# Kernel tuning notes

Hardware: AMD Instinct MI355X
Metric: run time of the kernel (lower is better)

## Reference

```python
import jax, jax.numpy as jnp
import numpy as np

NEG = -9e15

def setup_inputs() -> dict:
    key = jax.random.key(0)
    k1, k2, k3, k4 = jax.random.split(key, 4)
    N, F_IN, F_OUT = 8192, 256, 256
    h = jax.random.normal(k1, (N, F_IN), dtype=jnp.float32)
    adj = jax.random.randint(k2, (N, N), 0, 2, dtype=jnp.int32)
    W = jax.random.normal(k3, (F_IN, F_OUT), dtype=jnp.float32) * (1.0 / np.sqrt(F_IN))
    a = jax.random.normal(k4, (2 * F_OUT,), dtype=jnp.float32) * (1.0 / np.sqrt(2 * F_OUT))
    return {"h": h, "adj": adj, "W": W, "a": a}

def reference(h, adj, W, a):
    # Wh: [N, F_out]
    Wh = h @ W
    F_OUT = Wh.shape[1]
    a1, a2 = a[:F_OUT], a[F_OUT:]
    # cat-based score decomposes: e_ij = leaky_relu(a1.Wh_i + a2.Wh_j)
    s1 = Wh @ a1  # [N]
    s2 = Wh @ a2  # [N]
    e = jax.nn.leaky_relu(s1[:, None] + s2[None, :], negative_slope=0.2)  # [N, N]
    e = jnp.where(adj > 0, e, NEG)
    attention = jax.nn.softmax(e, axis=-1)
    # dropout is identity in eval mode
    return attention @ Wh
```

## Files before the change

kernel.cpp:

```cpp
#include <hip/hip_runtime.h>

typedef short s8v  __attribute__((ext_vector_type(8)));
typedef float f4v  __attribute__((ext_vector_type(4)));
typedef int   v4i  __attribute__((ext_vector_type(4)));
typedef float v4f  __attribute__((ext_vector_type(4)));

#define NNODES 8192
#define FDIM   256
#define NJC    4
#define JLEN   2048
#define TROWS  64
#define KSTEP  32
#define NSTEP  64

__device__ __forceinline__ float bf2f(unsigned short u) {
    unsigned int x = ((unsigned int)u) << 16;
    return __builtin_bit_cast(float, x);
}
__device__ __forceinline__ unsigned short f2bf(float f) {
    unsigned int x = __builtin_bit_cast(unsigned int, f);
    x += 0x7fffu + ((x >> 16) & 1u);
    return (unsigned short)(x >> 16);
}

__global__ __launch_bounds__(256) void wt_kernel(const float* __restrict__ W,
                                                 unsigned short* __restrict__ WT) {
    int idx = blockIdx.x * 256 + threadIdx.x;
    int r = idx >> 8, c = idx & 255;
    WT[c * 256 + r] = f2bf(W[r * 256 + c]);
}

__global__ __launch_bounds__(256) void wv_kernel(const float* __restrict__ W,
                                                 const float* __restrict__ a,
                                                 float* __restrict__ v1, float* __restrict__ v2) {
    __shared__ float r1[256], r2[256];
    int b = blockIdx.x, n = threadIdx.x;
    float w = W[(size_t)b * FDIM + n];
    r1[n] = w * a[n];
    r2[n] = w * a[FDIM + n];
    __syncthreads();
    for (int off = 128; off > 0; off >>= 1) {
        if (n < off) { r1[n] += r1[n + off]; r2[n] += r2[n + off]; }
        __syncthreads();
    }
    if (n == 0) { v1[b] = r1[0]; v2[b] = r2[0]; }
}

__global__ __launch_bounds__(256) void wh_kernel(
    const float* __restrict__ h, const unsigned short* __restrict__ WT,
    const float* __restrict__ v1, const float* __restrict__ v2,
    unsigned short* __restrict__ PB,
    float* __restrict__ s1, float* __restrict__ s2)
{
    __shared__ float v1_lds[FDIM], v2_lds[FDIM];
    int tid = threadIdx.x;
    v1_lds[tid] = v1[tid];
    v2_lds[tid] = v2[tid];
    __syncthreads();

    int w = tid >> 6, lane = tid & 63, q = lane >> 4, l15 = lane & 15;
    int i_base = blockIdx.x * 64 + w * 16;

    f4v acc[16] = {};
    float s1p = 0.f, s2p = 0.f;

    for (int k0 = 0; k0 < 256; k0 += 32) {
        const float* hp = h + (size_t)(i_base + l15) * FDIM + k0 + q * 8;
        f4v h0 = *(const f4v*)hp;
        f4v h1 = *(const f4v*)(hp + 4);
        s8v af;
#pragma unroll
        for (int j = 0; j < 4; ++j) {
            af[j]     = (short)f2bf(h0[j]);
            af[4 + j] = (short)f2bf(h1[j]);
            s1p += h0[j] * v1_lds[k0 + q * 8 + j] + h1[j] * v1_lds[k0 + q * 8 + 4 + j];
            s2p += h0[j] * v2_lds[k0 + q * 8 + j] + h1[j] * v2_lds[k0 + q * 8 + 4 + j];
        }
#pragma unroll
        for (int t = 0; t < 16; ++t) {
            s8v bf = *(const s8v*)(WT + (size_t)(t * 16 + l15) * FDIM + k0 + q * 8);
            acc[t] = __builtin_amdgcn_mfma_f32_16x16x32_bf16(af, bf, acc[t], 0, 0, 0);
        }
    }

    s1p += __shfl_xor(s1p, 16, 64);
    s1p += __shfl_xor(s1p, 32, 64);
    s2p += __shfl_xor(s2p, 16, 64);
    s2p += __shfl_xor(s2p, 32, 64);
    if (lane < 16) {
        s1[i_base + lane] = s1p;
        s2[i_base + lane] = s2p;
    }

#pragma unroll
    for (int t = 0; t < 16; ++t)
#pragma unroll
        for (int r = 0; r < 4; ++r) {
            int i = i_base + q * 4 + r;
            size_t a16 = (size_t)((i >> 5) * 16 + t) * 512
                       + l15 * 32 + ((i >> 3) & 3) * 8 + (i & 7);
            PB[a16] = f2bf(acc[t][r]);
        }
}

__global__ __launch_bounds__(256, 3) void attn_partial(
    const int* __restrict__ adj, const unsigned short* __restrict__ PB,
    const float* __restrict__ s1, const float* __restrict__ s2,
    float* __restrict__ Npart, float* __restrict__ dpart)
{
    __shared__ float s2_lds[JLEN];
    __shared__ unsigned short P_lds[2][TROWS * KSTEP];
    __shared__ float dsum_lds[TROWS][4];

    int tid = threadIdx.x;
    int rt = blockIdx.x & 127, jc = blockIdx.x >> 7;
    int j0 = jc * JLEN;

    for (int i = tid; i < JLEN / 4; i += 256)
        ((v4f*)s2_lds)[i] = ((const v4f*)(s2 + j0))[i];

    int m = tid >> 2, idx = tid & 3;
    int row_g = rt * TROWS + m;
    float s1v = s1[row_g];
    const int* arow = adj + (size_t)row_g * NNODES + j0 + idx * 8;
    int woff = ((idx * 64 + m) * 8) ^ (idx * 16);

    int g = tid >> 6, lane = tid & 63, q = lane >> 4, l15 = lane & 15;
    const unsigned short* pbb = PB + (size_t)(jc * 64) * 16 * 512 + l15 * 32 + q * 8;

    f4v acc[4][4] = {};
    float dsum = 0.0f;

    __syncthreads();

    v4i a0 = __builtin_nontemporal_load((const v4i*)(arow));
    v4i a1 = __builtin_nontemporal_load((const v4i*)(arow + 4));
    v4i cur0 = __builtin_nontemporal_load((const v4i*)(arow + KSTEP));
    v4i cur1 = __builtin_nontemporal_load((const v4i*)(arow + KSTEP + 4));
    {
        int kb = idx * 8;
        v4f sA = *(const v4f*)&s2_lds[kb];
        v4f sB = *(const v4f*)&s2_lds[kb + 4];
        s8v pv;
#pragma unroll
        for (int j = 0; j < 4; ++j) {
            float x = s1v + sA[j];
            float p = (a0[j] > 0) ? __expf(fmaxf(x, 0.2f * x)) : 0.0f;
            unsigned short pb = f2bf(p);
            pv[j] = (short)pb; dsum += bf2f(pb);
            float x2 = s1v + sB[j];
            float p2 = (a1[j] > 0) ? __expf(fmaxf(x2, 0.2f * x2)) : 0.0f;
            unsigned short pb2 = f2bf(p2);
            pv[4 + j] = (short)pb2; dsum += bf2f(pb2);
        }
        *(s8v*)&P_lds[0][woff] = pv;
    }
    __syncthreads();

    for (int s = 0; s < NSTEP; ++s) {
        int kn = (s < NSTEP - 2) ? (s + 2) * KSTEP : 0;
        v4i nx0 = __builtin_nontemporal_load((const v4i*)(arow + kn));
        v4i nx1 = __builtin_nontemporal_load((const v4i*)(arow + kn + 4));

        s8v bf[4];
#pragma unroll
        for (int t = 0; t < 4; ++t)
            bf[t] = *(const s8v*)(pbb + (size_t)(s * 16 + g * 4 + t) * 512);

        if (s < NSTEP - 1) {
            int kb = (s + 1) * KSTEP + idx * 8;
            v4f sA = *(const v4f*)&s2_lds[kb];
            v4f sB = *(const v4f*)&s2_lds[kb + 4];
            s8v pv;
#pragma unroll
            for (int j = 0; j < 4; ++j) {
                float x = s1v + sA[j];
                float p = (cur0[j] > 0) ? __expf(fmaxf(x, 0.2f * x)) : 0.0f;
                unsigned short pb = f2bf(p);
                pv[j] = (short)pb; dsum += bf2f(pb);
                float x2 = s1v + sB[j];
                float p2 = (cur1[j] > 0) ? __expf(fmaxf(x2, 0.2f * x2)) : 0.0f;
                unsigned short pb2 = f2bf(p2);
                pv[4 + j] = (short)pb2; dsum += bf2f(pb2);
            }
            *(s8v*)&P_lds[(s + 1) & 1][woff] = pv;
        }

        const unsigned short* pbuf = P_lds[s & 1];
#pragma unroll
        for (int rh = 0; rh < 4; ++rh) {
            s8v af = *(const s8v*)&pbuf[((q * 64 + rh * 16 + l15) * 8) ^ (q * 16)];
#pragma unroll
            for (int t = 0; t < 4; ++t)
                acc[rh][t] = __builtin_amdgcn_mfma_f32_16x16x32_bf16(af, bf[t], acc[rh][t], 0, 0, 0);
        }

        __syncthreads();
        cur0 = nx0; cur1 = nx1;
    }

    dsum_lds[m][idx] = dsum;
    __syncthreads();
    if (tid < TROWS) {
        float d = dsum_lds[tid][0] + dsum_lds[tid][1] + dsum_lds[tid][2] + dsum_lds[tid][3];
        dpart[jc * NNODES + rt * TROWS + tid] = d;
    }

#pragma unroll
    for (int rh = 0; rh < 4; ++rh)
#pragma unroll
        for (int r = 0; r < 4; ++r) {
            int row = rh * 16 + q * 4 + r;
            float* base = Npart + ((size_t)(jc * NNODES) + rt * TROWS + row) * FDIM;
#pragma unroll
            for (int t = 0; t < 4; ++t)
                __builtin_nontemporal_store(acc[rh][t][r], base + g * 64 + t * 16 + l15);
        }
}

__global__ __launch_bounds__(256) void reduce_kernel(
    const float* __restrict__ Npart, const float* __restrict__ dpart,
    float* __restrict__ out)
{
    int i = blockIdx.x, n = threadIdx.x;
    float d = 0.f, acc = 0.f;
#pragma unroll
    for (int jc = 0; jc < NJC; ++jc) {
        d += dpart[jc * NNODES + i];
        acc += Npart[((size_t)(jc * NNODES) + i) * FDIM + n];
    }
    out[(size_t)i * FDIM + n] = acc / fmaxf(d, 1e-30f);
}

extern "C" void kernel_launch(void* const* d_in, const int* in_sizes, int n_in,
                              void* d_out, int out_size, void* d_ws, size_t ws_size,
                              hipStream_t stream) {
    const float* h   = (const float*)d_in[0];
    const int*   adj = (const int*)d_in[1];
    const float* W   = (const float*)d_in[2];
    const float* a   = (const float*)d_in[3];
    float* out = (float*)d_out;

    char* ws = (char*)d_ws;
    unsigned short* PB = (unsigned short*)ws;
    float* s1 = (float*)(ws + (4u << 20));
    float* s2 = (float*)(ws + (4u << 20) + (32u << 10));
    unsigned short* WT = (unsigned short*)(ws + (4u << 20) + (64u << 10));
    float* v1 = (float*)(ws + (4u << 20) + (192u << 10));
    float* v2 = (float*)(ws + (4u << 20) + (193u << 10));
    float* dpart = (float*)(ws + (5u << 20));
    float* Npart = (float*)(ws + (8u << 20));

    hipLaunchKernelGGL(wt_kernel, dim3(256), dim3(256), 0, stream, W, WT);
    hipLaunchKernelGGL(wv_kernel, dim3(256), dim3(256), 0, stream, W, a, v1, v2);
    hipLaunchKernelGGL(wh_kernel, dim3(128), dim3(256), 0, stream, h, WT, v1, v2, PB, s1, s2);
    hipLaunchKernelGGL(attn_partial, dim3(128 * NJC), dim3(256), 0, stream,
                       adj, PB, s1, s2, Npart, dpart);
    hipLaunchKernelGGL(reduce_kernel, dim3(NNODES), dim3(256), 0, stream, Npart, dpart, out);
}
```

Measured before the change: 447.0 us.

## Use packed bf16 conversion, split j-range into 8 chunks, raise occupancy

Replaces the manual round-to-nearest bf16 conversion with the hardware packed v_cvt_pk_bf16_f32 instruction in both the projection and attention kernels, and writes PB as packed 2x32-bit stores. The attention kernel now splits the column range into 8 chunks of 1024 instead of 4 of 2048, reorders the block index so neighbouring blocks share a row tile, and raises launch bounds to 4 blocks per SM. The denominator now sums unrounded fp32 probabilities, so it no longer matches the bf16 values fed to the MFMA exactly. More j-chunks also mean more partial results to reduce later, and the unseen reduction code must handle NJC=8.

Measured after the change: 466.8 us. 1.04x slower.

```diff
diff --git a/kernel.cpp b/kernel.cpp
--- a/kernel.cpp
+++ b/kernel.cpp
@@ -4,14 +4,15 @@
 typedef float f4v  __attribute__((ext_vector_type(4)));
 typedef int   v4i  __attribute__((ext_vector_type(4)));
 typedef float v4f  __attribute__((ext_vector_type(4)));
+typedef int   v2i  __attribute__((ext_vector_type(2)));
 
 #define NNODES 8192
 #define FDIM   256
-#define NJC    4
-#define JLEN   2048
+#define NJC    8
+#define JLEN   1024
 #define TROWS  64
 #define KSTEP  32
-#define NSTEP  64
+#define NSTEP  32
 
 __device__ __forceinline__ float bf2f(unsigned short u) {
     unsigned int x = ((unsigned int)u) << 16;
@@ -21,6 +22,11 @@
     unsigned int x = __builtin_bit_cast(unsigned int, f);
     x += 0x7fffu + ((x >> 16) & 1u);
     return (unsigned short)(x >> 16);
+}
+__device__ __forceinline__ int cvt_pk(float lo, float hi) {
+    int r;
+    asm("v_cvt_pk_bf16_f32 %0, %1, %2" : "=v"(r) : "v"(lo), "v"(hi));
+    return r;
 }
 
 __global__ __launch_bounds__(256) void wt_kernel(const float* __restrict__ W,
@@ -68,18 +74,20 @@
         const float* hp = h + (size_t)(i_base + l15) * FDIM + k0 + q * 8;
         f4v h0 = *(const f4v*)hp;
         f4v h1 = *(const f4v*)(hp + 4);
-        s8v af;
+        union { v4i u; s8v s; } af;
+        af.u[0] = cvt_pk(h0[0], h0[1]);
+        af.u[1] = cvt_pk(h0[2], h0[3]);
+        af.u[2] = cvt_pk(h1[0], h1[1]);
+        af.u[3] = cvt_pk(h1[2], h1[3]);
 #pragma unroll
         for (int j = 0; j < 4; ++j) {
-            af[j]     = (short)f2bf(h0[j]);
-            af[4 + j] = (short)f2bf(h1[j]);
             s1p += h0[j] * v1_lds[k0 + q * 8 + j] + h1[j] * v1_lds[k0 + q * 8 + 4 + j];
             s2p += h0[j] * v2_lds[k0 + q * 8 + j] + h1[j] * v2_lds[k0 + q * 8 + 4 + j];
         }
 #pragma unroll
         for (int t = 0; t < 16; ++t) {
             s8v bf = *(const s8v*)(WT + (size_t)(t * 16 + l15) * FDIM + k0 + q * 8);
-            acc[t] = __builtin_amdgcn_mfma_f32_16x16x32_bf16(af, bf, acc[t], 0, 0, 0);
+            acc[t] = __builtin_amdgcn_mfma_f32_16x16x32_bf16(af.s, bf, acc[t], 0, 0, 0);
         }
     }
 
@@ -93,17 +101,18 @@
     }
 
 #pragma unroll
-    for (int t = 0; t < 16; ++t)
-#pragma unroll
-        for (int r = 0; r < 4; ++r) {
-            int i = i_base + q * 4 + r;
-            size_t a16 = (size_t)((i >> 5) * 16 + t) * 512
-                       + l15 * 32 + ((i >> 3) & 3) * 8 + (i & 7);
-            PB[a16] = f2bf(acc[t][r]);
-        }
-}
-
-__global__ __launch_bounds__(256, 3) void attn_partial(
+    for (int t = 0; t < 16; ++t) {
+        int i0 = i_base + q * 4;
+        size_t a16 = (size_t)((i0 >> 5) * 16 + t) * 512
+                   + l15 * 32 + ((i0 >> 3) & 3) * 8 + (i0 & 7);
+        v2i pk;
+        pk[0] = cvt_pk(acc[t][0], acc[t][1]);
+        pk[1] = cvt_pk(acc[t][2], acc[t][3]);
+        *(v2i*)(PB + a16) = pk;
+    }
+}
+
+__global__ __launch_bounds__(256, 4) void attn_partial(
     const int* __restrict__ adj, const unsigned short* __restrict__ PB,
     const float* __restrict__ s1, const float* __restrict__ s2,
     float* __restrict__ Npart, float* __restrict__ dpart)
@@ -113,7 +122,7 @@
     __shared__ float dsum_lds[TROWS][4];
 
     int tid = threadIdx.x;
-    int rt = blockIdx.x & 127, jc = blockIdx.x >> 7;
+    int jc = blockIdx.x & 7, rt = blockIdx.x >> 3;
     int j0 = jc * JLEN;
 
     for (int i = tid; i < JLEN / 4; i += 256)
@@ -126,7 +135,7 @@
     int woff = ((idx * 64 + m) * 8) ^ (idx * 16);
 
     int g = tid >> 6, lane = tid & 63, q = lane >> 4, l15 = lane & 15;
-    const unsigned short* pbb = PB + (size_t)(jc * 64) * 16 * 512 + l15 * 32 + q * 8;
+    const unsigned short* pbb = PB + (size_t)(jc * 32) * 16 * 512 + l15 * 32 + q * 8;
 
     f4v acc[4][4] = {};
     float dsum = 0.0f;
@@ -141,19 +150,22 @@
         int kb = idx * 8;
         v4f sA = *(const v4f*)&s2_lds[kb];
         v4f sB = *(const v4f*)&s2_lds[kb + 4];
-        s8v pv;
+        float pa[4], pb_[4];
 #pragma unroll
         for (int j = 0; j < 4; ++j) {
             float x = s1v + sA[j];
             float p = (a0[j] > 0) ? __expf(fmaxf(x, 0.2f * x)) : 0.0f;
-            unsigned short pb = f2bf(p);
-            pv[j] = (short)pb; dsum += bf2f(pb);
+            pa[j] = p; dsum += p;
             float x2 = s1v + sB[j];
             float p2 = (a1[j] > 0) ? __expf(fmaxf(x2, 0.2f * x2)) : 0.0f;
-            unsigned short pb2 = f2bf(p2);
-            pv[4 + j] = (short)pb2; dsum += bf2f(pb2);
-        }
-        *(s8v*)&P_lds[0][woff] = pv;
+            pb_[j] = p2; dsum += p2;
+        }
+        v4i pv;
+        pv[0] = cvt_pk(pa[0], pa[1]);
+        pv[1] = cvt_pk(pa[2], pa[3]);
+        pv[2] = cvt_pk(pb_[0], pb_[1]);
+        pv[3] = cvt_pk(pb_[2], pb_[3]);
+        *(v4i*)&P_lds[0][woff] = pv;
     }
     __syncthreads();
 
@@ -171,19 +183,22 @@
             int kb = (s + 1) * KSTEP + idx * 8;
             v4f sA = *(const v4f*)&s2_lds[kb];
             v4f sB = *(const v4f*)&s2_lds[kb + 4];
-            s8v pv;
+            float pa[4], pb_[4];
 #pragma unroll
             for (int j = 0; j < 4; ++j) {
                 float x = s1v + sA[j];
                 float p = (cur0[j] > 0) ? __expf(fmaxf(x, 0.2f * x)) : 0.0f;
-                unsigned short pb = f2bf(p);
-                pv[j] = (short)pb; dsum += bf2f(pb);
+                pa[j] = p; dsum += p;
                 float x2 = s1v + sB[j];
                 float p2 = (cur1[j] > 0) ? __expf(fmaxf(x2, 0.2f * x2)) : 0.0f;
-                unsigned short pb2 = f2bf(p2);
-                pv[4 + j] = (short)pb2; dsum += bf2f(pb2);
+                pb_[j] = p2; dsum += p2;
             }
-            *(s8v*)&P_lds[(s + 1) & 1][woff] = pv;
+            v4i pv;
+            pv[0] = cvt_pk(pa[0], pa[1]);
+            pv[1] = cvt_pk(pa[2], pa[3]);
+            pv[2] = cvt_pk(pb_[0], pb_[1]);
+            pv[3] = cvt_pk(pb_[2], pb_[3]);
+            *(v4i*)&P_lds[(s + 1) & 1][woff] = pv;
         }
 
         const unsigned short* pbuf = P_lds[s & 1];
```
